# Optimization experiments

Hardware: AMD Instinct MI355X
Metric: run time of the kernel (lower is better)

The kernel has to match this reference:

```python
import jax, jax.numpy as jnp
import numpy as np

HID = 768
NH = 12
HD = HID // NH
EPS = 1e-12


def _layernorm(x, g, b):
    m = x.mean(-1, keepdims=True)
    v = ((x - m) ** 2).mean(-1, keepdims=True)
    return (x - m) / jnp.sqrt(v + EPS) * g + b


def _mha_block(x, mask, Wq, bq, Wk, bk, Wv, bv, Wo, bo, ln_g, ln_b):
    # x: [B,S,H]; mask broadcastable to [B,NH,S,S] (additive)
    B, S, _ = x.shape
    split = lambda t: t.reshape(B, S, NH, HD).transpose(0, 2, 1, 3)  # [B,NH,S,HD]
    q = split(x @ Wq + bq)
    k = split(x @ Wk + bk)
    v = split(x @ Wv + bv)
    scores = jnp.einsum('bhqd,bhkd->bhqk', q, k) / np.float32(np.sqrt(HD)) + mask
    probs = jax.nn.softmax(scores, axis=-1)
    ctx = jnp.einsum('bhqk,bhkd->bhqd', probs, v)
    ctx = ctx.transpose(0, 2, 1, 3).reshape(B, S, HID)
    # BertSelfOutput: dense + residual + LayerNorm
    return _layernorm(ctx @ Wo + bo + x, ln_g, ln_b)


def setup_inputs() -> dict:
    key = jax.random.key(0)
    ks = jax.random.split(key, 32)
    B, S = 32, 512
    scale = 0.02
    W = lambda i, di, do: jax.random.normal(ks[i], (di, do), jnp.float32) * scale
    inp = {
        'hidden_states': jax.random.normal(ks[0], (B, S, HID), jnp.float32),
        'attention_mask': jnp.zeros((B, 1, 1, S), jnp.float32),
        # token-level attention params
        'Wq': W(1, HID, HID), 'bq': jnp.zeros((HID,), jnp.float32),
        'Wk': W(2, HID, HID), 'bk': jnp.zeros((HID,), jnp.float32),
        'Wv': W(3, HID, HID), 'bv': jnp.zeros((HID,), jnp.float32),
        'Wao': W(4, HID, HID), 'bao': jnp.zeros((HID,), jnp.float32),
        'ln1_g': jnp.ones((HID,), jnp.float32), 'ln1_b': jnp.zeros((HID,), jnp.float32),
        # dialog (CLS-level) attention params
        'dWq': W(5, HID, HID), 'dbq': jnp.zeros((HID,), jnp.float32),
        'dWk': W(6, HID, HID), 'dbk': jnp.zeros((HID,), jnp.float32),
        'dWv': W(7, HID, HID), 'dbv': jnp.zeros((HID,), jnp.float32),
        'dWo': W(8, HID, HID), 'dbo': jnp.zeros((HID,), jnp.float32),
        'dln_g': jnp.ones((HID,), jnp.float32), 'dln_b': jnp.zeros((HID,), jnp.float32),
        # FFN params
        'Wi': W(9, HID, 4 * HID), 'bi': jnp.zeros((4 * HID,), jnp.float32),
        'Wo2': W(10, 4 * HID, HID), 'bo2': jnp.zeros((HID,), jnp.float32),
        'ln2_g': jnp.ones((HID,), jnp.float32), 'ln2_b': jnp.zeros((HID,), jnp.float32),
        'turns': 8,
    }
    return inp


def reference(hidden_states, attention_mask,
              Wq, bq, Wk, bk, Wv, bv, Wao, bao, ln1_g, ln1_b,
              dWq, dbq, dWk, dbk, dWv, dbv, dWo, dbo, dln_g, dln_b,
              Wi, bi, Wo2, bo2, ln2_g, ln2_b, turns):
    # 1) token-level self-attention + SelfOutput
    x = _mha_block(hidden_states, attention_mask,
                   Wq, bq, Wk, bk, Wv, bv, Wao, bao, ln1_g, ln1_b)
    # 2) hierarchical dialog attention over per-turn CLS tokens
    bs = x.shape[0] // turns
    cls = x[:, 0].reshape(bs, turns, HID)
    pos = jnp.arange(turns)
    # faithful to source: (j >= i) -> -10000 (masks diagonal and future)
    cmask = (pos[None, :] >= pos[:, None]).astype(x.dtype) * (-10000.0)
    cmask = cmask[None, None, :, :]  # broadcast to [bs, NH, turns, turns]
    cls = _mha_block(cls, cmask, dWq, dbq, dWk, dbk, dWv, dbv, dWo, dbo, dln_g, dln_b)
    x = x.at[:, 0].set(cls.reshape(-1, HID))
    # 3) FFN: intermediate (gelu) + output dense + residual + LayerNorm
    inter = jax.nn.gelu(x @ Wi + bi, approximate=False)
    out = _layernorm(inter @ Wo2 + bo2 + x, ln2_g, ln2_b)
    return out
```

## Files before the change

### kernel.cpp

```cpp
#include <hip/hip_runtime.h>
#include <hip/hip_bf16.h>
#include <math.h>

using bf16 = __hip_bfloat16;
typedef __attribute__((ext_vector_type(8))) __bf16 bf16x8;
typedef __attribute__((ext_vector_type(4))) __bf16 bf16x4;
typedef __attribute__((ext_vector_type(4))) float f32x4;

__device__ __forceinline__ float b2f(bf16 x){ return __bfloat162float(x); }
__device__ __forceinline__ bf16  f2b(float x){ return __float2bfloat16(x); }
__device__ __forceinline__ float ldf(const float* p, size_t i){ return p[i]; }
__device__ __forceinline__ float ldf(const bf16*  p, size_t i){ return b2f(p[i]); }
__device__ __forceinline__ void stf(float* p, size_t i, float v){ p[i] = v; }
__device__ __forceinline__ void stf(bf16*  p, size_t i, float v){ p[i] = f2b(v); }

__device__ __forceinline__ void st4(float* p, float a, float b, float c, float d){
  float4 f; f.x=a; f.y=b; f.z=c; f.w=d; *(float4*)p = f;
}
__device__ __forceinline__ void st4(bf16* p, float a, float b, float c, float d){
  bf16x4 o; o[0]=(__bf16)a; o[1]=(__bf16)b; o[2]=(__bf16)c; o[3]=(__bf16)d;
  *(bf16x4*)p = o;
}

__device__ __forceinline__ float gelu_f(float v){
  float u = v*(0.7978845608f + 0.0356774081f*v*v);
  float e = __expf(2.f*u);
  float t = 1.f - 2.f/(e+1.f);
  return 0.5f*v*(1.f+t);
}

typedef const __attribute__((address_space(1))) unsigned int* gas_u32p;
typedef __attribute__((address_space(3))) unsigned int* las_u32p;
__device__ __forceinline__ void gl_lds16(const bf16* g, bf16* l){
  __builtin_amdgcn_global_load_lds((gas_u32p)(const void*)g, (las_u32p)(void*)l, 16, 0, 0);
}

#define MFMA16 __builtin_amdgcn_mfma_f32_16x16x32_bf16

#define LGKM(N) do { \
  asm volatile("s_waitcnt lgkmcnt(" #N ")" ::: "memory"); \
  __builtin_amdgcn_sched_barrier(0); \
} while(0)

#define NHEAD 12
#define HDIM  64
#define HID   768
#define SEQ   512
#define BATCH 32
#define ROWS  (BATCH*SEQ)
#define QKVW  2304
#define QCH   128
#define NCHUNK (SEQ/QCH)
#define FT    128

template<int EPI, typename TR>
__global__ __launch_bounds__(512,2)
void gemm8p(const bf16* __restrict__ A, int lda,
            const bf16* __restrict__ Bt, int ldb,
            bf16* __restrict__ C, int ldc, int K,
            const float* __restrict__ bias,
            const TR* __restrict__ res, int ldres)
{
  __shared__ __align__(16) bf16 tileLds[4][256*64];

  const int tid  = threadIdx.x;
  const int wave = tid>>6, lane = tid&63;
  const int r = lane&15, qd = lane>>4;
  const int wr = wave>>2, wc = wave&3;
  const int m0 = blockIdx.y*256, n0 = blockIdx.x*256;
  const int NTK = K>>6;
  const int wbase = wave*512;

  const int sr = tid>>3, sp = tid&7;
  const bf16* pA = A  + (size_t)(m0+sr)*lda + ((sp^(sr&7))<<3);
  const bf16* pB = Bt + (size_t)(n0+sr)*ldb + ((sp^(sr&7))<<3);

  auto stage = [&](int H){
    const int u = H>>2, idx = H&3, bufi = u&1;
    const size_t kof = (size_t)u*64;
    if (idx==0){
      gl_lds16(pA + kof,                    tileLds[bufi*2] + wbase);
      gl_lds16(pA + kof + (size_t)64*lda,   tileLds[bufi*2] + wbase + 4096);
    } else if (idx==3){
      gl_lds16(pA + kof + (size_t)128*lda,  tileLds[bufi*2] + 8192 + wbase);
      gl_lds16(pA + kof + (size_t)192*lda,  tileLds[bufi*2] + 8192 + wbase + 4096);
    } else {
      const int h = idx-1;
      gl_lds16(pB + kof + (size_t)(h*128)*ldb,
               tileLds[bufi*2+1] + h*8192 + wbase);
      gl_lds16(pB + kof + (size_t)(h*128+64)*ldb,
               tileLds[bufi*2+1] + h*8192 + wbase + 4096);
    }
  };

  auto rdA = [&](const bf16* base, int mi, int ks)->bf16x8{
    const int row = mi*32 + wr*16 + r;
    return *(const bf16x8*)(base + row*64 + ((((ks<<2)|qd) ^ (r&7))<<3));
  };
  auto rdB = [&](const bf16* base, int nj, int ks)->bf16x8{
    const int row = nj*64 + wc*16 + r;
    return *(const bf16x8*)(base + row*64 + ((((ks<<2)|qd) ^ (r&7))<<3));
  };

  #pragma unroll
  for (int H=0; H<7; ++H) stage(H);
  asm volatile("s_waitcnt vmcnt(6)" ::: "memory");
  __builtin_amdgcn_s_barrier();

  f32x4 acc[8][4] = {};

  for (int t=0; t<NTK; ++t){
    const bf16* a = tileLds[(t&1)*2];
    const bf16* b = tileLds[(t&1)*2+1];
    const int Hb = 4*t + 6;
    const int Hmax = 4*NTK;
    bf16x8 af[4][2], bn0[2][2], bn1[2][2];

    af[0][0]=rdA(a,0,0); af[0][1]=rdA(a,0,1);
    af[1][0]=rdA(a,1,0); af[1][1]=rdA(a,1,1);
    bn0[0][0]=rdB(b,0,0); bn0[0][1]=rdB(b,0,1);
    bn0[1][0]=rdB(b,1,0); bn0[1][1]=rdB(b,1,1);
    __builtin_amdgcn_sched_barrier(0);
    af[2][0]=rdA(a,2,0); af[2][1]=rdA(a,2,1);
    af[3][0]=rdA(a,3,0); af[3][1]=rdA(a,3,1);
    if (Hb+1 < Hmax) stage(Hb+1);
    LGKM(4);
    __builtin_amdgcn_s_setprio(1);
    #pragma unroll
    for (int mi=0;mi<2;mi++)
      #pragma unroll
      for (int nj=0;nj<2;nj++){
        acc[mi][nj] = MFMA16(af[mi][0], bn0[nj][0], acc[mi][nj],0,0,0);
        acc[mi][nj] = MFMA16(af[mi][1], bn0[nj][1], acc[mi][nj],0,0,0);
      }
    LGKM(0);
    #pragma unroll
    for (int mi=2;mi<4;mi++)
      #pragma unroll
      for (int nj=0;nj<2;nj++){
        acc[mi][nj] = MFMA16(af[mi][0], bn0[nj][0], acc[mi][nj],0,0,0);
        acc[mi][nj] = MFMA16(af[mi][1], bn0[nj][1], acc[mi][nj],0,0,0);
      }
    __builtin_amdgcn_s_setprio(0);
    __builtin_amdgcn_s_barrier();

    bn1[0][0]=rdB(b,2,0); bn1[0][1]=rdB(b,2,1);
    __builtin_amdgcn_sched_barrier(0);
    bn1[1][0]=rdB(b,3,0); bn1[1][1]=rdB(b,3,1);
    if (Hb+2 < Hmax) stage(Hb+2);
    LGKM(2);
    __builtin_amdgcn_s_setprio(1);
    #pragma unroll
    for (int mi=0;mi<4;mi++){
      acc[mi][2] = MFMA16(af[mi][0], bn1[0][0], acc[mi][2],0,0,0);
      acc[mi][2] = MFMA16(af[mi][1], bn1[0][1], acc[mi][2],0,0,0);
    }
    LGKM(0);
    #pragma unroll
    for (int mi=0;mi<4;mi++){
      acc[mi][3] = MFMA16(af[mi][0], bn1[1][0], acc[mi][3],0,0,0);
      acc[mi][3] = MFMA16(af[mi][1], bn1[1][1], acc[mi][3],0,0,0);
    }
    __builtin_amdgcn_s_setprio(0);
    __builtin_amdgcn_s_barrier();

    af[0][0]=rdA(a,4,0); af[0][1]=rdA(a,4,1);
    af[1][0]=rdA(a,5,0); af[1][1]=rdA(a,5,1);
    __builtin_amdgcn_sched_barrier(0);
    af[2][0]=rdA(a,6,0); af[2][1]=rdA(a,6,1);
    af[3][0]=rdA(a,7,0); af[3][1]=rdA(a,7,1);
    if (Hb+3 < Hmax) stage(Hb+3);
    LGKM(4);
    __builtin_amdgcn_s_setprio(1);
    #pragma unroll
    for (int mi=0;mi<2;mi++)
      #pragma unroll
      for (int nj=0;nj<2;nj++){
        acc[4+mi][2+nj] = MFMA16(af[mi][0], bn1[nj][0], acc[4+mi][2+nj],0,0,0);
        acc[4+mi][2+nj] = MFMA16(af[mi][1], bn1[nj][1], acc[4+mi][2+nj],0,0,0);
      }
    LGKM(0);
    #pragma unroll
    for (int mi=2;mi<4;mi++)
      #pragma unroll
      for (int nj=0;nj<2;nj++){
        acc[4+mi][2+nj] = MFMA16(af[mi][0], bn1[nj][0], acc[4+mi][2+nj],0,0,0);
        acc[4+mi][2+nj] = MFMA16(af[mi][1], bn1[nj][1], acc[4+mi][2+nj],0,0,0);
      }
    __builtin_amdgcn_s_setprio(0);
    __builtin_amdgcn_s_barrier();

    if (Hb+4 < Hmax) stage(Hb+4);
    __builtin_amdgcn_s_setprio(1);
    #pragma unroll
    for (int mi=0;mi<4;mi++)
      #pragma unroll
      for (int nj=0;nj<2;nj++){
        acc[4+mi][nj] = MFMA16(af[mi][0], bn0[nj][0], acc[4+mi][nj],0,0,0);
        acc[4+mi][nj] = MFMA16(af[mi][1], bn0[nj][1], acc[4+mi][nj],0,0,0);
      }
    __builtin_amdgcn_s_setprio(0);
    if (t < NTK-2) { asm volatile("s_waitcnt vmcnt(6)" ::: "memory"); }
    else           { asm volatile("s_waitcnt vmcnt(0)" ::: "memory"); }
    __builtin_amdgcn_s_barrier();
  }

  float bs[4];
  #pragma unroll
  for (int nj=0;nj<4;nj++)
    bs[nj] = bias ? bias[n0 + nj*64 + wc*16 + r] : 0.f;
  #pragma unroll
  for (int mi=0;mi<8;mi++){
    #pragma unroll
    for (int nj=0;nj<4;nj++){
      #pragma unroll
      for (int i=0;i<4;i++){
        const int mm = m0 + mi*32 + wr*16 + qd*4 + i;
        const int nn = n0 + nj*64 + wc*16 + r;
        float v = acc[mi][nj][i] + bs[nj];
        if (EPI==1) v = gelu_f(v);
        if (EPI==2) v += ldf(res, (size_t)mm*ldres + nn);
        C[(size_t)mm*ldc + nn] = f2b(v);
      }
    }
  }
}

__global__ __launch_bounds__(256)
void flash_attn(const bf16* __restrict__ qkv, const bf16* __restrict__ vtb,
                const float* __restrict__ mask, bf16* __restrict__ ctx)
{
  const int qc = blockIdx.x;
  const int z  = blockIdx.y;
  const int b  = z / NHEAD, h = z - b*NHEAD;
  const int q0 = qc*QCH;

  __shared__ __align__(16) bf16 Ks[FT*64];
  __shared__ __align__(16) bf16 Vts[64*FT];
  __shared__ __align__(16) bf16 Ps[QCH*64];

  const int tid = threadIdx.x;
  const int wave = tid>>6, lane = tid&63;
  const int r = lane&15, qd = lane>>4;
  const int wr = wave;

  const bf16* Qg = qkv + ((size_t)(b*SEQ + q0))*QKVW + h*HDIM;
  const bf16* Kg = qkv + ((size_t)b*SEQ)*QKVW + 768 + h*HDIM;
  const bf16* Vg = vtb + (size_t)z*HDIM*SEQ;

  auto stageK = [&](int k0){
    #pragma unroll
    for (int c0=0;c0<1024;c0+=256){
      int c = c0+tid, row = c>>3, pos = c&7;
      gl_lds16(Kg + (size_t)(k0+row)*QKVW + ((pos^(row&7))*8),
               Ks + (size_t)(c0 + wave*64)*8);
    }
  };
  auto stageV = [&](int k0){
    #pragma unroll
    for (int c0=0;c0<1024;c0+=256){
      int c = c0+tid, row = c>>4, pos = c&15;
      gl_lds16(Vg + (size_t)row*SEQ + k0 + ((pos^(row&7))*8),
               Vts + (size_t)(c0 + wave*64)*8);
    }
  };

  stageK(0);
  stageV(0);
  bf16x8 qf[2][2];
  #pragma unroll
  for (int mi=0;mi<2;mi++)
    #pragma unroll
    for (int ks=0;ks<2;ks++)
      qf[mi][ks] = *(const bf16x8*)(Qg + (size_t)(wr*32+mi*16+r)*QKVW + (ks*4+qd)*8);

  f32x4 accO[2][4] = {};
  float mrun[2][4], lrun[2][4];
  #pragma unroll
  for (int a=0;a<2;a++)
    #pragma unroll
    for (int i2=0;i2<4;i2++){ mrun[a][i2]=-1e30f; lrun[a][i2]=0.f; }

  for (int k0=0; k0<SEQ; k0+=FT){
    __syncthreads();

    float mk[8];
    #pragma unroll
    for (int ni=0;ni<8;ni++)
      mk[ni] = mask[(size_t)b*SEQ + k0 + ni*16 + r];

    f32x4 accS[2][8] = {};
    #pragma unroll
    for (int ks=0; ks<2; ks++){
      bf16x8 bfv[8];
      #pragma unroll
      for (int ni=0;ni<8;ni++){
        int row = ni*16 + r;
        int jr = ks*4 + qd;
        bfv[ni] = *(const bf16x8*)(Ks + row*64 + ((jr^(row&7))*8));
      }
      #pragma unroll
      for (int mi=0;mi<2;mi++)
        #pragma unroll
        for (int ni=0;ni<8;ni++)
          accS[mi][ni] = MFMA16(qf[mi][ks], bfv[ni], accS[mi][ni], 0,0,0);
    }

    __syncthreads();
    if (k0+FT < SEQ) stageK(k0+FT);

    #pragma unroll
    for (int mi=0;mi<2;mi++){
      #pragma unroll
      for (int i=0;i<4;i++){
        float mx = -1e30f;
        #pragma unroll
        for (int ni=0;ni<8;ni++){
          float v = accS[mi][ni][i]*0.125f + mk[ni];
          accS[mi][ni][i] = v;
          mx = fmaxf(mx, v);
        }
        #pragma unroll
        for (int off=1; off<16; off<<=1) mx = fmaxf(mx, __shfl_xor(mx, off));
        float mnew = fmaxf(mrun[mi][i], mx);
        float alpha = __expf(mrun[mi][i] - mnew);
        mrun[mi][i] = mnew;
        float ssum = 0.f;
        #pragma unroll
        for (int ni=0;ni<8;ni++){
          float p = __expf(accS[mi][ni][i] - mnew);
          accS[mi][ni][i] = p;
          ssum += p;
        }
        #pragma unroll
        for (int off=1; off<16; off<<=1) ssum += __shfl_xor(ssum, off);
        lrun[mi][i] = lrun[mi][i]*alpha + ssum;
        #pragma unroll
        for (int ni=0;ni<4;ni++) accO[mi][ni][i] *= alpha;
      }
    }

    #pragma unroll
    for (int half=0; half<2; half++){
      #pragma unroll
      for (int mi=0;mi<2;mi++){
        #pragma unroll
        for (int i=0;i<4;i++){
          int row = wr*32 + mi*16 + qd*4 + i;
          #pragma unroll
          for (int nj=0;nj<4;nj++){
            int colL = nj*16 + r;
            int chunk = colL>>3;
            Ps[row*64 + ((chunk^(row&7))*8) + (colL&7)] = f2b(accS[mi][half*4+nj][i]);
          }
        }
      }
      #pragma unroll
      for (int ks=0; ks<2; ks++){
        bf16x8 af[2], bfv[4];
        #pragma unroll
        for (int mi=0;mi<2;mi++){
          int row = wr*32 + mi*16 + r;
          int jr = ks*4 + qd;
          af[mi] = *(const bf16x8*)(Ps + row*64 + ((jr^(row&7))*8));
        }
        #pragma unroll
        for (int ni=0;ni<4;ni++){
          int row = ni*16 + r;
          int jrv = half*8 + ks*4 + qd;
          bfv[ni] = *(const bf16x8*)(Vts + row*FT + ((jrv^(row&7))*8));
        }
        #pragma unroll
        for (int mi=0;mi<2;mi++)
          #pragma unroll
          for (int ni=0;ni<4;ni++)
            accO[mi][ni] = MFMA16(af[mi], bfv[ni], accO[mi][ni], 0,0,0);
      }
    }

    __syncthreads();
    if (k0+FT < SEQ) stageV(k0+FT);
  }

  bf16* Cg = ctx + ((size_t)(b*SEQ + q0))*HID + h*HDIM;
  #pragma unroll
  for (int mi=0;mi<2;mi++)
    #pragma unroll
    for (int i=0;i<4;i++){
      int row = wr*32 + mi*16 + qd*4 + i;
      float invl = 1.0f/lrun[mi][i];
      #pragma unroll
      for (int ni=0;ni<4;ni++)
        Cg[(size_t)row*HID + ni*16 + r] = f2b(accO[mi][ni][i]*invl);
    }
}

__global__ void transpose_cast(const float* __restrict__ in, bf16* __restrict__ out,
                               int R, int C)
{
  __shared__ float tile[32][33];
  int bc = blockIdx.x*32, br = blockIdx.y*32;
  int tx = threadIdx.x, ty = threadIdx.y;
  #pragma unroll
  for (int i=ty;i<32;i+=8)
    tile[i][tx] = in[(size_t)(br+i)*C + bc+tx];
  __syncthreads();
  #pragma unroll
  for (int i=ty;i<32;i+=8)
    out[(size_t)(bc+i)*R + br+tx] = f2b(tile[tx][i]);
}

__global__ void transpose_cast4(const float* __restrict__ w0, const float* __restrict__ w1,
                                const float* __restrict__ w2, const float* __restrict__ w3,
                                bf16* __restrict__ out)
{
  const float* in = blockIdx.z==0?w0 : blockIdx.z==1?w1 : blockIdx.z==2?w2 : w3;
  bf16* o = out + (size_t)blockIdx.z*768*768;
  __shared__ float tile[32][33];
  int bc = blockIdx.x*32, br = blockIdx.y*32;
  int tx = threadIdx.x, ty = threadIdx.y;
  #pragma unroll
  for (int i=ty;i<32;i+=8)
    tile[i][tx] = in[(size_t)(br+i)*768 + bc+tx];
  __syncthreads();
  #pragma unroll
  for (int i=ty;i<32;i+=8)
    o[(size_t)(bc+i)*768 + br+tx] = f2b(tile[tx][i]);
}

__global__ __launch_bounds__(256)
void castX(const float* __restrict__ in, bf16* __restrict__ out)
{
  int i = blockIdx.x*256 + threadIdx.x;
  float4 f = ((const float4*)in)[i];
  union{ unsigned long long u; __bf16 h[4]; } pk;
  pk.h[0]=(__bf16)f.x; pk.h[1]=(__bf16)f.y; pk.h[2]=(__bf16)f.z; pk.h[3]=(__bf16)f.w;
  ((unsigned long long*)out)[i] = pk.u;
}

__global__ void concat_bias(const float* __restrict__ a, const float* __restrict__ b,
                            const float* __restrict__ c, float* __restrict__ o)
{
  int i = blockIdx.x*256 + threadIdx.x;
  if (i < 768) o[i] = a[i];
  else if (i < 1536) o[i] = b[i-768];
  else if (i < 2304) o[i] = c[i-1536];
}

__global__ void vtrans(const bf16* __restrict__ v, bf16* __restrict__ vt)
{
  int z = blockIdx.z; int b = z/NHEAD, h = z - b*NHEAD;
  int d0 = blockIdx.x*32, s0 = blockIdx.y*32;
  __shared__ bf16 t[32][33];
  int tx = threadIdx.x, ty = threadIdx.y;
  #pragma unroll
  for (int i=ty;i<32;i+=8)
    t[i][tx] = v[(size_t)(b*SEQ + s0+i)*QKVW + h*HDIM + d0+tx];
  __syncthreads();
  #pragma unroll
  for (int i=ty;i<32;i+=8)
    vt[(size_t)z*HDIM*SEQ + (size_t)(d0+i)*SEQ + s0+tx] = t[tx][i];
}

template<typename TO>
__global__ __launch_bounds__(256)
void ln768(const bf16* __restrict__ y, const float* __restrict__ g,
           const float* __restrict__ be, TO* __restrict__ dst)
{
  const int wave = threadIdx.x>>6, lane = threadIdx.x&63;
  const size_t row = (size_t)blockIdx.x*4 + wave;
  const bf16* yr = y + row*HID;
  float x[12];
  float s = 0.f, q = 0.f;
  #pragma unroll
  for (int c=0;c<3;c++){
    bf16x4 v = *(const bf16x4*)(yr + c*256 + lane*4);
    #pragma unroll
    for (int j=0;j<4;j++){
      float f = (float)v[j];
      x[c*4+j] = f;
      s += f; q += f*f;
    }
  }
  #pragma unroll
  for (int off=1; off<64; off<<=1){ s += __shfl_xor(s, off); q += __shfl_xor(q, off); }
  float mean = s*(1.0f/HID);
  float var  = q*(1.0f/HID) - mean*mean;
  float inv  = rsqrtf(var + 1e-12f);
  TO* dr = dst + row*HID;
  #pragma unroll
  for (int c=0;c<3;c++){
    float4 gg = *(const float4*)(g  + c*256 + lane*4);
    float4 bb = *(const float4*)(be + c*256 + lane*4);
    st4(dr + c*256 + lane*4,
        (x[c*4+0]-mean)*inv*gg.x + bb.x,
        (x[c*4+1]-mean)*inv*gg.y + bb.y,
        (x[c*4+2]-mean)*inv*gg.z + bb.z,
        (x[c*4+3]-mean)*inv*gg.w + bb.w);
  }
}

__global__ __launch_bounds__(256)
void cls_proj(const bf16* __restrict__ x2,
              const float* __restrict__ Wq, const float* __restrict__ bq,
              const float* __restrict__ Wk, const float* __restrict__ bk,
              const float* __restrict__ Wv, const float* __restrict__ bv,
              bf16* __restrict__ oq, bf16* __restrict__ ok, bf16* __restrict__ ov)
{
  int mat = blockIdx.x, row = blockIdx.y;
  const float* W  = mat==0 ? Wq : (mat==1 ? Wk : Wv);
  const float* bi = mat==0 ? bq : (mat==1 ? bk : bv);
  bf16* out       = mat==0 ? oq : (mat==1 ? ok : ov);
  __shared__ float a[HID];
  const bf16* xr = x2 + (size_t)row*SEQ*HID;
  for (int i=threadIdx.x;i<HID;i+=256) a[i] = b2f(xr[i]);
  __syncthreads();
  for (int c0=0;c0<HID;c0+=256){
    int col = c0 + threadIdx.x;
    float acc = 0.f;
    for (int k=0;k<HID;k++) acc += a[k]*W[(size_t)k*HID + col];
    out[(size_t)row*HID + col] = f2b(acc + bi[col]);
  }
}

__global__ __launch_bounds__(64)
void cls_attn(const bf16* __restrict__ q, const bf16* __restrict__ k,
              const bf16* __restrict__ v, bf16* __restrict__ ctx)
{
  int z = blockIdx.x; int bb = z/NHEAD, h = z - bb*NHEAD;
  __shared__ float P[8][8];
  int t = threadIdx.x;
  int qi = t>>3, ki = t&7;
  float s = 0.f;
  for (int d=0; d<HDIM; d++)
    s += b2f(q[(size_t)(bb*8+qi)*HID + h*HDIM + d]) *
         b2f(k[(size_t)(bb*8+ki)*HID + h*HDIM + d]);
  s = s*0.125f + (ki >= qi ? -10000.0f : 0.0f);
  float m = s;
  #pragma unroll
  for (int off=4; off; off>>=1) m = fmaxf(m, __shfl_xor(m, off, 8));
  float e = __expf(s - m);
  float sum = e;
  #pragma unroll
  for (int off=4; off; off>>=1) sum += __shfl_xor(sum, off, 8);
  P[qi][ki] = e/sum;
  __syncthreads();
  for (int q2=0; q2<8; q2++){
    float acc = 0.f;
    #pragma unroll
    for (int k2=0; k2<8; k2++)
      acc += P[q2][k2] * b2f(v[(size_t)(bb*8+k2)*HID + h*HDIM + t]);
    ctx[(size_t)(bb*8+q2)*HID + h*HDIM + t] = f2b(acc);
  }
}

__global__ __launch_bounds__(256)
void cls_out(const bf16* __restrict__ ctx, const float* __restrict__ Wo,
             const float* __restrict__ bo, const float* __restrict__ g,
             const float* __restrict__ be, bf16* __restrict__ x2)
{
  int row = blockIdx.x;
  __shared__ float a[HID];
  __shared__ float yrow[HID];
  const bf16* cr = ctx + (size_t)row*HID;
  bf16* xr = x2 + (size_t)row*SEQ*HID;
  for (int i=threadIdx.x;i<HID;i+=256) a[i] = b2f(cr[i]);
  __syncthreads();
  for (int c0=0;c0<HID;c0+=256){
    int col = c0 + threadIdx.x;
    float acc = 0.f;
    for (int k=0;k<HID;k++) acc += a[k]*Wo[(size_t)k*HID + col];
    yrow[col] = acc + bo[col] + b2f(xr[col]);
  }
  __syncthreads();
  int t = threadIdx.x;
  float x0 = yrow[t], x1 = yrow[t+256], x2v = yrow[t+512];
  float s = x0+x1+x2v, qq = x0*x0+x1*x1+x2v*x2v;
  #pragma unroll
  for (int off=32; off; off>>=1){ s += __shfl_xor(s, off); qq += __shfl_xor(qq, off); }
  __shared__ float rs[4], rq[4];
  int wv = t>>6;
  if ((t&63)==0){ rs[wv]=s; rq[wv]=qq; }
  __syncthreads();
  s = rs[0]+rs[1]+rs[2]+rs[3];
  qq = rq[0]+rq[1]+rq[2]+rq[3];
  float mean = s*(1.0f/HID);
  float var  = qq*(1.0f/HID) - mean*mean;
  float inv  = rsqrtf(var + 1e-12f);
  xr[t    ] = f2b((x0 -mean)*inv*g[t    ] + be[t    ]);
  xr[t+256] = f2b((x1 -mean)*inv*g[t+256] + be[t+256]);
  xr[t+512] = f2b((x2v-mean)*inv*g[t+512] + be[t+512]);
}

extern "C" void kernel_launch(void* const* d_in, const int* in_sizes, int n_in,
                              void* d_out, int out_size, void* d_ws, size_t ws_size,
                              hipStream_t stream)
{
  const float* X    = (const float*)d_in[0];
  const float* AM   = (const float*)d_in[1];
  const float* Wq   = (const float*)d_in[2];  const float* bq  = (const float*)d_in[3];
  const float* Wk   = (const float*)d_in[4];  const float* bk  = (const float*)d_in[5];
  const float* Wv   = (const float*)d_in[6];  const float* bv  = (const float*)d_in[7];
  const float* Wao  = (const float*)d_in[8];  const float* bao = (const float*)d_in[9];
  const float* ln1g = (const float*)d_in[10]; const float* ln1b= (const float*)d_in[11];
  const float* dWq  = (const float*)d_in[12]; const float* dbq = (const float*)d_in[13];
  const float* dWk  = (const float*)d_in[14]; const float* dbk = (const float*)d_in[15];
  const float* dWv  = (const float*)d_in[16]; const float* dbv = (const float*)d_in[17];
  const float* dWo  = (const float*)d_in[18]; const float* dbo = (const float*)d_in[19];
  const float* dlng = (const float*)d_in[20]; const float* dlnb= (const float*)d_in[21];
  const float* Wi   = (const float*)d_in[22]; const float* bi  = (const float*)d_in[23];
  const float* Wo2  = (const float*)d_in[24]; const float* bo2 = (const float*)d_in[25];
  const float* ln2g = (const float*)d_in[26]; const float* ln2b= (const float*)d_in[27];
  float* OUT = (float*)d_out;

  char* wp = (char*)d_ws;
  auto alloc = [&](size_t elems)->bf16*{
    bf16* p = (bf16*)wp;
    wp += ((elems*sizeof(bf16) + 255)/256)*256;
    return p;
  };
  bf16* wtq  = alloc(768*768);
  bf16* wtk  = alloc(768*768);
  bf16* wtv  = alloc(768*768);
  bf16* wtao = alloc(768*768);
  bf16* wti  = alloc((size_t)768*3072);
  bf16* wto2 = alloc((size_t)3072*768);
  float* bqkv = (float*)alloc(2304*2);
  bf16* qkv  = alloc((size_t)ROWS*QKVW);
  bf16* vtb  = alloc((size_t)ROWS*HID);
  bf16* inter = qkv;
  bf16* scb  = alloc((size_t)ROWS*HID);
  bf16* yb   = scb;
  bf16* x2   = scb;
  bf16* ctxb = alloc((size_t)ROWS*HID);
  bf16* xb   = ctxb;
  bf16* clsq = alloc(32*HID);
  bf16* clsk = alloc(32*HID);
  bf16* clsv = alloc(32*HID);
  bf16* clsc = alloc(32*HID);
  (void)wtk; (void)wtv;

  dim3 T32(32,8);
  transpose_cast4<<<dim3(24,24,4), T32, 0, stream>>>(Wq, Wk, Wv, Wao, wtq);
  transpose_cast<<<dim3(96,24), T32, 0, stream>>>(Wi,  wti, 768, 3072);
  transpose_cast<<<dim3(24,96), T32, 0, stream>>>(Wo2, wto2,3072, 768);
  concat_bias<<<9,256,0,stream>>>(bq, bk, bv, bqkv);
  castX<<<ROWS*HID/4/256,256,0,stream>>>(X, xb);

  gemm8p<0,float><<<dim3(9,64),512,0,stream>>>(
      xb,768,  wtq,768,  qkv,QKVW, 768, bqkv, (const float*)nullptr, 0);

  vtrans<<<dim3(2,16,BATCH*NHEAD), T32, 0, stream>>>(qkv + 1536, vtb);

  flash_attn<<<dim3(NCHUNK, BATCH*NHEAD),256,0,stream>>>(qkv, vtb, AM, ctxb);

  gemm8p<2,float><<<dim3(3,64),512,0,stream>>>(
      ctxb,768,  wtao,768,  yb,768, 768, bao, X, 768);
  ln768<bf16><<<ROWS/4,256,0,stream>>>(yb, ln1g, ln1b, x2);

  cls_proj<<<dim3(3,32),256,0,stream>>>(x2, dWq,dbq, dWk,dbk, dWv,dbv,
                                        clsq, clsk, clsv);
  cls_attn<<<48,64,0,stream>>>(clsq, clsk, clsv, clsc);
  cls_out<<<32,256,0,stream>>>(clsc, dWo, dbo, dlng, dlnb, x2);

  gemm8p<1,float><<<dim3(12,64),512,0,stream>>>(
      x2,768,  wti,768,  inter,3072, 768, bi, (const float*)nullptr, 0);
  gemm8p<2,bf16><<<dim3(3,64),512,0,stream>>>(
      inter,3072,  wto2,3072,  yb,768, 3072, bo2, x2, 768);
  ln768<float><<<ROWS/4,256,0,stream>>>(yb, ln2g, ln2b, OUT);
}
```

Baseline: 822.1 us.

## Rework flash attention to 32x32 MFMA with transposed S and register-resident P

The attention kernel now computes S^T with 32x32x16 MFMAs, so each lane owns one query row. Softmax row reductions shrink to a single cross-half shuffle, and the probabilities are packed to bf16 with permlane32 swaps and fed straight into the PV MFMA, removing the LDS round trip through the P buffer. The mask is preloaded into LDS pre-scaled by 8 and used as the initial accumulator, and the output stores become packed 8-byte writes. The cost is higher register pressure from the 16-wide accumulators, plus reliance on gfx950-specific instructions.

```diff
diff --git a/kernel.cpp b/kernel.cpp
--- a/kernel.cpp
+++ b/kernel.cpp
@@ -6,6 +6,8 @@
 typedef __attribute__((ext_vector_type(8))) __bf16 bf16x8;
 typedef __attribute__((ext_vector_type(4))) __bf16 bf16x4;
 typedef __attribute__((ext_vector_type(4))) float f32x4;
+typedef __attribute__((ext_vector_type(16))) float f32x16;
+typedef unsigned int u32x2 __attribute__((ext_vector_type(2)));
 
 __device__ __forceinline__ float b2f(bf16 x){ return __bfloat162float(x); }
 __device__ __forceinline__ bf16  f2b(float x){ return __float2bfloat16(x); }
@@ -36,11 +38,22 @@
 }
 
 #define MFMA16 __builtin_amdgcn_mfma_f32_16x16x32_bf16
+#define MFMA32 __builtin_amdgcn_mfma_f32_32x32x16_bf16
 
 #define LGKM(N) do { \
   asm volatile("s_waitcnt lgkmcnt(" #N ")" ::: "memory"); \
   __builtin_amdgcn_sched_barrier(0); \
 } while(0)
+
+__device__ __forceinline__ unsigned cvtpk(float lo, float hi){
+  unsigned w;
+  asm("v_cvt_pk_bf16_f32 %0, %1, %2" : "=v"(w) : "v"(lo), "v"(hi));
+  return w;
+}
+__device__ __forceinline__ void plswap(unsigned &a, unsigned &b){
+  u32x2 r = __builtin_amdgcn_permlane32_swap(a, b, false, false);
+  a = r[0]; b = r[1];
+}
 
 #define NHEAD 12
 #define HDIM  64
@@ -237,11 +250,11 @@
 
   __shared__ __align__(16) bf16 Ks[FT*64];
   __shared__ __align__(16) bf16 Vts[64*FT];
-  __shared__ __align__(16) bf16 Ps[QCH*64];
+  __shared__ __align__(16) float smask[FT];
 
   const int tid = threadIdx.x;
   const int wave = tid>>6, lane = tid&63;
-  const int r = lane&15, qd = lane>>4;
+  const int l31 = lane&31, hi = lane>>5;
   const int wr = wave;
 
   const bf16* Qg = qkv + ((size_t)(b*SEQ + q0))*QKVW + h*HDIM;
@@ -267,132 +280,119 @@
 
   stageK(0);
   stageV(0);
-  bf16x8 qf[2][2];
-  #pragma unroll
-  for (int mi=0;mi<2;mi++)
-    #pragma unroll
-    for (int ks=0;ks<2;ks++)
-      qf[mi][ks] = *(const bf16x8*)(Qg + (size_t)(wr*32+mi*16+r)*QKVW + (ks*4+qd)*8);
-
-  f32x4 accO[2][4] = {};
-  float mrun[2][4], lrun[2][4];
-  #pragma unroll
-  for (int a=0;a<2;a++)
-    #pragma unroll
-    for (int i2=0;i2<4;i2++){ mrun[a][i2]=-1e30f; lrun[a][i2]=0.f; }
+  if (tid < FT) smask[tid] = 8.0f*mask[(size_t)b*SEQ + tid];
+  bf16x8 qf[4];
+  #pragma unroll
+  for (int hs=0;hs<4;hs++)
+    qf[hs] = *(const bf16x8*)(Qg + (size_t)(wr*32+l31)*QKVW + hs*16 + hi*8);
+
+  f32x16 accO[2] = {};
+  float mrun = -1e30f, lrun = 0.f;
 
   for (int k0=0; k0<SEQ; k0+=FT){
     __syncthreads();
 
-    float mk[8];
-    #pragma unroll
-    for (int ni=0;ni<8;ni++)
-      mk[ni] = mask[(size_t)b*SEQ + k0 + ni*16 + r];
-
-    f32x4 accS[2][8] = {};
-    #pragma unroll
-    for (int ks=0; ks<2; ks++){
-      bf16x8 bfv[8];
-      #pragma unroll
-      for (int ni=0;ni<8;ni++){
-        int row = ni*16 + r;
-        int jr = ks*4 + qd;
-        bfv[ni] = *(const bf16x8*)(Ks + row*64 + ((jr^(row&7))*8));
-      }
-      #pragma unroll
-      for (int mi=0;mi<2;mi++)
-        #pragma unroll
-        for (int ni=0;ni<8;ni++)
-          accS[mi][ni] = MFMA16(qf[mi][ks], bfv[ni], accS[mi][ni], 0,0,0);
+    f32x16 S[4];
+    #pragma unroll
+    for (int kb=0;kb<4;kb++){
+      #pragma unroll
+      for (int rq=0;rq<4;rq++){
+        f32x4 mq = *(const f32x4*)(smask + kb*32 + rq*8 + hi*4);
+        S[kb][rq*4+0]=mq[0]; S[kb][rq*4+1]=mq[1];
+        S[kb][rq*4+2]=mq[2]; S[kb][rq*4+3]=mq[3];
+      }
+    }
+    #pragma unroll
+    for (int hs=0;hs<4;hs++){
+      bf16x8 kf[4];
+      #pragma unroll
+      for (int kb=0;kb<4;kb++){
+        int row = kb*32 + l31;
+        int ch  = hs*2 + hi;
+        kf[kb] = *(const bf16x8*)(Ks + row*64 + ((ch^(row&7))*8));
+      }
+      #pragma unroll
+      for (int kb=0;kb<4;kb++)
+        S[kb] = MFMA32(kf[kb], qf[hs], S[kb], 0,0,0);
     }
 
     __syncthreads();
     if (k0+FT < SEQ) stageK(k0+FT);
 
-    #pragma unroll
-    for (int mi=0;mi<2;mi++){
-      #pragma unroll
-      for (int i=0;i<4;i++){
-        float mx = -1e30f;
+    float mx = -1e30f;
+    #pragma unroll
+    for (int kb=0;kb<4;kb++)
+      #pragma unroll
+      for (int e=0;e<16;e++){
+        float v = S[kb][e]*0.125f;
+        S[kb][e] = v;
+        mx = fmaxf(mx, v);
+      }
+    mx = fmaxf(mx, __shfl_xor(mx, 32));
+    float mnew = fmaxf(mrun, mx);
+    float alpha = __expf(mrun - mnew);
+    mrun = mnew;
+    float ps = 0.f;
+    #pragma unroll
+    for (int kb=0;kb<4;kb++)
+      #pragma unroll
+      for (int e=0;e<16;e++){
+        float p = __expf(S[kb][e] - mnew);
+        S[kb][e] = p;
+        ps += p;
+      }
+    ps += __shfl_xor(ps, 32);
+    lrun = lrun*alpha + ps;
+    #pragma unroll
+    for (int dt=0;dt<2;dt++)
+      #pragma unroll
+      for (int e=0;e<16;e++)
+        accO[dt][e] *= alpha;
+
+    #pragma unroll
+    for (int kb=0;kb<4;kb++){
+      unsigned w[8];
+      #pragma unroll
+      for (int m=0;m<8;m++)
+        w[m] = cvtpk(S[kb][2*m], S[kb][2*m+1]);
+      plswap(w[0], w[2]);  plswap(w[1], w[3]);
+      plswap(w[4], w[6]);  plswap(w[5], w[7]);
+      union { unsigned u[4]; bf16x8 v; } pf0, pf1;
+      pf0.u[0]=w[0]; pf0.u[1]=w[1]; pf0.u[2]=w[2]; pf0.u[3]=w[3];
+      pf1.u[0]=w[4]; pf1.u[1]=w[5]; pf1.u[2]=w[6]; pf1.u[3]=w[7];
+      #pragma unroll
+      for (int ks2=0;ks2<2;ks2++){
+        const bf16x8 pf = ks2 ? pf1.v : pf0.v;
         #pragma unroll
-        for (int ni=0;ni<8;ni++){
-          float v = accS[mi][ni][i]*0.125f + mk[ni];
-          accS[mi][ni][i] = v;
-          mx = fmaxf(mx, v);
+        for (int dt=0;dt<2;dt++){
+          int row = dt*32 + l31;
+          int ch  = kb*4 + ks2*2 + hi;
+          bf16x8 vf = *(const bf16x8*)(Vts + row*FT + ((ch^(row&7))*8));
+          accO[dt] = MFMA32(vf, pf, accO[dt], 0,0,0);
         }
-        #pragma unroll
-        for (int off=1; off<16; off<<=1) mx = fmaxf(mx, __shfl_xor(mx, off));
-        float mnew = fmaxf(mrun[mi][i], mx);
-        float alpha = __expf(mrun[mi][i] - mnew);
-        mrun[mi][i] = mnew;
-        float ssum = 0.f;
-        #pragma unroll
-        for (int ni=0;ni<8;ni++){
-          float p = __expf(accS[mi][ni][i] - mnew);
-          accS[mi][ni][i] = p;
-          ssum += p;
-        }
-        #pragma unroll
-        for (int off=1; off<16; off<<=1) ssum += __shfl_xor(ssum, off);
-        lrun[mi][i] = lrun[mi][i]*alpha + ssum;
-        #pragma unroll
-        for (int ni=0;ni<4;ni++) accO[mi][ni][i] *= alpha;
-      }
-    }
-
-    #pragma unroll
-    for (int half=0; half<2; half++){
-      #pragma unroll
-      for (int mi=0;mi<2;mi++){
-        #pragma unroll
-        for (int i=0;i<4;i++){
-          int row = wr*32 + mi*16 + qd*4 + i;
-          #pragma unroll
-          for (int nj=0;nj<4;nj++){
-            int colL = nj*16 + r;
-            int chunk = colL>>3;
-            Ps[row*64 + ((chunk^(row&7))*8) + (colL&7)] = f2b(accS[mi][half*4+nj][i]);
-          }
-        }
-      }
-      #pragma unroll
-      for (int ks=0; ks<2; ks++){
-        bf16x8 af[2], bfv[4];
-        #pragma unroll
-        for (int mi=0;mi<2;mi++){
-          int row = wr*32 + mi*16 + r;
-          int jr = ks*4 + qd;
-          af[mi] = *(const bf16x8*)(Ps + row*64 + ((jr^(row&7))*8));
-        }
-        #pragma unroll
-        for (int ni=0;ni<4;ni++){
-          int row = ni*16 + r;
-          int jrv = half*8 + ks*4 + qd;
-          bfv[ni] = *(const bf16x8*)(Vts + row*FT + ((jrv^(row&7))*8));
-        }
-        #pragma unroll
-        for (int mi=0;mi<2;mi++)
-          #pragma unroll
-          for (int ni=0;ni<4;ni++)
-            accO[mi][ni] = MFMA16(af[mi], bfv[ni], accO[mi][ni], 0,0,0);
       }
     }
 
     __syncthreads();
-    if (k0+FT < SEQ) stageV(k0+FT);
-  }
-
-  bf16* Cg = ctx + ((size_t)(b*SEQ + q0))*HID + h*HDIM;
-  #pragma unroll
-  for (int mi=0;mi<2;mi++)
-    #pragma unroll
-    for (int i=0;i<4;i++){
-      int row = wr*32 + mi*16 + qd*4 + i;
-      float invl = 1.0f/lrun[mi][i];
-      #pragma unroll
-      for (int ni=0;ni<4;ni++)
-        Cg[(size_t)row*HID + ni*16 + r] = f2b(accO[mi][ni][i]*invl);
-    }
+    if (k0+FT < SEQ){
+      stageV(k0+FT);
+      if (tid < FT) smask[tid] = 8.0f*mask[(size_t)b*SEQ + k0+FT + tid];
+    }
+  }
+
+  float invl = 1.0f/lrun;
+  bf16* Cg = ctx + ((size_t)(b*SEQ + q0 + wr*32 + l31))*HID + h*HDIM;
+  #pragma unroll
+  for (int dt=0;dt<2;dt++){
+    #pragma unroll
+    for (int rq=0;rq<4;rq++){
+      union { unsigned long long u; __bf16 hh[4]; } pk;
+      #pragma unroll
+      for (int i=0;i<4;i++)
+        pk.hh[i] = (__bf16)(accO[dt][rq*4+i]*invl);
+      *(unsigned long long*)(Cg + dt*32 + rq*8 + hi*4) = pk.u;
+    }
+  }
 }
 
 __global__ void transpose_cast(const float* __restrict__ in, bf16* __restrict__ out,
```

Result: no change. 813.1 us (-1.1%).
